# Optimization experiments

Measured on AMD Instinct MI355X. Metric: run time of the kernel, lower is better.

The kernel has to match this reference:

```python
import jax, jax.numpy as jnp
import numpy as np

BS = 15
NA = BS * BS
NOISE_SCALE = 2.0
TEMP = 0.03
VALUE_NOISE = 200.0

def _build_windows():
    # all length-5 windows in the 4 directions of a 15x15 board (572 total)
    wins = []
    for dr, dc in ((0, 1), (1, 0), (1, 1), (1, -1)):
        for r in range(BS):
            for c in range(BS):
                er, ec = r + 4 * dr, c + 4 * dc
                if 0 <= er < BS and 0 <= ec < BS:
                    wins.append([(r + k * dr) * BS + (c + k * dc) for k in range(5)])
    return np.asarray(wins, dtype=np.int32)

_WIN = _build_windows()                      # [572, 5] flat cell indices
_NW = _WIN.shape[0]
_Mnp = np.zeros((NA, _NW), dtype=np.float32)  # membership: cell i in window w
for w in range(_NW):
    _Mnp[_WIN[w], w] = 1.0
WIN_CELLS = jnp.asarray(_WIN)
MEMBER = jnp.asarray(_Mnp)                   # [225, 572]
WEIGHTS = jnp.asarray([0.0, 5.0, 50.0, 500.0, 5000.0, 100000.0], dtype=jnp.float32)

def _window_score(pc, oc):
    # matches _eval_board's per-window scoring table
    sp = jnp.where((oc == 0) & (pc > 0), WEIGHTS[jnp.minimum(pc, 5)], 0.0)
    so = jnp.where((pc == 0) & (oc > 0), WEIGHTS[jnp.minimum(oc, 5)], 0.0)
    return sp - so

def setup_inputs() -> dict:
    key = jax.random.key(0)
    k1, k2, k3, k4 = jax.random.split(key, 4)
    B = 8192
    boards = jax.random.randint(k1, (B, NA), 0, 3, dtype=jnp.int32)
    current_player = jax.random.randint(k2, (B,), 1, 3, dtype=jnp.int32)
    policy_noise = jax.random.normal(k3, (B, NA), dtype=jnp.float32)
    value_noise = jax.random.normal(k4, (B,), dtype=jnp.float32)
    return {"boards": boards, "current_player": current_player,
            "policy_noise": policy_noise, "value_noise": value_noise}

def reference(boards, current_player, policy_noise, value_noise):
    player = current_player[:, None, None]           # [B,1,1]
    opp = 3 - player
    cells = boards[:, WIN_CELLS]                      # [B, 572, 5]
    pc0 = jnp.sum(cells == player, axis=-1)           # [B, 572] player stones per window
    oc0 = jnp.sum(cells == opp, axis=-1)              # [B, 572] opponent stones per window
    s0 = _window_score(pc0, oc0)                      # base per-window score
    base = jnp.sum(s0, axis=-1)                       # [B] = _eval_board(board, player)
    # placing a player stone in an empty cell adds +1 to pc of every window containing it
    d = _window_score(pc0 + 1, oc0) - s0              # [B, 572]
    delta = jnp.einsum('bw,aw->ba', d, MEMBER)        # [B, 225]
    win_w = ((pc0 == 4) & (oc0 == 0)).astype(jnp.float32)
    win = jnp.einsum('bw,aw->ba', win_w, MEMBER) > 0  # [B, 225]
    empty = boards == 0
    logits = jnp.where(empty, jnp.where(win, 1e5, base[:, None] + delta), -1e6)
    valid = logits > -1e5                             # matches `logits > -100000.0`
    n = jnp.sum(valid, axis=-1).astype(jnp.float32)
    nsafe = jnp.maximum(n, 1.0)
    mean = jnp.sum(jnp.where(valid, logits, 0.0), axis=-1) / nsafe
    var = jnp.sum(jnp.where(valid, (logits - mean[:, None]) ** 2, 0.0), axis=-1) / nsafe
    std = jnp.maximum(1.0, jnp.sqrt(var))             # population std, floored at 1
    logits = logits + jnp.where(valid & (n[:, None] > 0),
                                policy_noise * NOISE_SCALE * std[:, None], 0.0)
    policy = jax.nn.softmax(logits * TEMP, axis=-1)   # [B, 225]
    value = jnp.clip(jnp.tanh((base + value_noise * VALUE_NOISE) / 3000.0), -0.95, 0.95)[:, None]
    return policy, value
```

## Files before the change

kernel.cpp:

```cpp
#include <hip/hip_runtime.h>
#include <math.h>

#define BSZ 15
#define NA  225
typedef unsigned long long u64;

__device__ __forceinline__ float wtab(int n) {
    return n == 1 ? 5.f : n == 2 ? 50.f : n == 3 ? 500.f : n == 4 ? 5000.f : 100000.f;
}
__device__ __forceinline__ float wredSum(float v) {
    #pragma unroll
    for (int off = 32; off; off >>= 1) v += __shfl_xor(v, off, 64);
    return v;
}
__device__ __forceinline__ float wredMax(float v) {
    #pragma unroll
    for (int off = 32; off; off >>= 1) v = fmaxf(v, __shfl_xor(v, off, 64));
    return v;
}

struct Masks { u64 P0, P1, P2, P3, O0, O1, O2, O3; };

template<int DIV, int CEXTRA, bool HAS64>
__device__ __forceinline__ void extractWin(int u, const Masks& M, u64 wmask,
                                           int& pc, int& oc)
{
    const int r = u / DIV;
    const int c = u % DIV + CEXTRA;
    const int idx = r * BSZ + c;
    const int q = idx >> 6, sh = idx & 63;
    const u64 Plo = (q & 2) ? ((q & 1) ? M.P3 : M.P2) : ((q & 1) ? M.P1 : M.P0);
    const u64 Phi = (q & 2) ? ((q & 1) ? 0ULL : M.P3) : ((q & 1) ? M.P2 : M.P1);
    const u64 Olo = (q & 2) ? ((q & 1) ? M.O3 : M.O2) : ((q & 1) ? M.O1 : M.O0);
    const u64 Ohi = (q & 2) ? ((q & 1) ? 0ULL : M.O3) : ((q & 1) ? M.O2 : M.O1);
    const u64 xP = (Plo >> sh) | ((Phi << (63 - sh)) << 1);
    const u64 xO = (Olo >> sh) | ((Ohi << (63 - sh)) << 1);
    pc = __popcll(xP & wmask);
    oc = __popcll(xO & wmask);
    if (HAS64) {
        pc += (int)((Phi >> sh) & 1ULL);
        oc += (int)((Ohi >> sh) & 1ULL);
    }
}

__device__ __forceinline__ void scoreD(int pc, int oc, float& s0, float& d) {
    const bool z_oc = (oc == 0), z_pc = (pc == 0);
    s0 = z_oc ? (z_pc ? 0.f : wtab(pc)) : (z_pc ? -wtab(oc) : 0.f);
    d  = (z_oc ? wtab(pc + 1) : 0.f) - s0;
}

__global__ __launch_bounds__(256, 4) void heur_kernel(
    const int* __restrict__ boards, const int* __restrict__ cur,
    const float* __restrict__ pnoise, const float* __restrict__ vnoise,
    float* __restrict__ out, int B)
{
    const int wid  = threadIdx.x >> 6;
    const int lane = threadIdx.x & 63;
    const int b    = blockIdx.x * 4 + wid;

    __shared__ float sDW[4][572];

    if (b >= B) return;

    float* __restrict__ dw = sDW[wid];

    const int player = cur[b];
    const int opp    = 3 - player;
    const int* __restrict__ gb = boards + (size_t)b * NA;

    const int v0 = gb[lane];
    const int v1 = gb[lane + 64];
    const int v2 = gb[lane + 128];
    const int v3 = (lane + 192 < NA) ? gb[lane + 192] : -1;

    const float* __restrict__ pn = pnoise + (size_t)b * NA;
    float pnv[4];
    pnv[0] = pn[lane];
    pnv[1] = pn[lane + 64];
    pnv[2] = pn[lane + 128];
    pnv[3] = (lane + 192 < NA) ? pn[lane + 192] : 0.f;
    const float vnb = vnoise[b];

    Masks M;
    M.P0 = __ballot(v0 == player); M.O0 = __ballot(v0 == opp);
    M.P1 = __ballot(v1 == player); M.O1 = __ballot(v1 == opp);
    M.P2 = __ballot(v2 == player); M.O2 = __ballot(v2 == opp);
    M.P3 = __ballot(v3 == player); M.O3 = __ballot(v3 == opp);

    const u64 MH = 0x1FULL;
    const u64 MV = 0x1000200040008001ULL;
    const u64 MD = 0x0001000100010001ULL;
    const u64 MA = 0x0100040010004001ULL;

    int pcS[10], ocS[10];
    const bool a2 = lane < 37, a7 = lane < 57;
    extractWin<11, 0, false>(lane,                 M, MH, pcS[0], ocS[0]);
    extractWin<11, 0, false>(lane + 64,            M, MH, pcS[1], ocS[1]);
    extractWin<11, 0, false>(min(lane + 128, 164), M, MH, pcS[2], ocS[2]);
    extractWin<15, 0, false>(lane,                 M, MV, pcS[3], ocS[3]);
    extractWin<15, 0, false>(lane + 64,            M, MV, pcS[4], ocS[4]);
    extractWin<15, 0, false>(min(lane + 128, 164), M, MV, pcS[5], ocS[5]);
    extractWin<11, 0, true >(lane,                 M, MD, pcS[6], ocS[6]);
    extractWin<11, 0, true >(min(lane + 64, 120),  M, MD, pcS[7], ocS[7]);
    extractWin<11, 4, false>(lane,                 M, MA, pcS[8], ocS[8]);
    extractWin<11, 4, false>(min(lane + 64, 120),  M, MA, pcS[9], ocS[9]);

    float baseLocal = 0.f;
    float s0v[10], dv[10];
    #pragma unroll
    for (int t = 0; t < 10; ++t) scoreD(pcS[t], ocS[t], s0v[t], dv[t]);
    const bool act[10] = {true, true, a2, true, true, a2, true, a7, true, a7};
    #pragma unroll
    for (int t = 0; t < 10; ++t) if (act[t]) baseLocal += s0v[t];

    dw[lane]             = dv[0];
    dw[lane + 64]        = dv[1];
    if (a2) dw[lane + 128] = dv[2];
    dw[165 + lane]       = dv[3];
    dw[165 + lane + 64]  = dv[4];
    if (a2) dw[165 + lane + 128] = dv[5];
    dw[330 + lane]       = dv[6];
    if (a7) dw[330 + lane + 64]  = dv[7];
    dw[451 + lane]       = dv[8];
    if (a7) dw[451 + lane + 64]  = dv[9];

    __threadfence_block();

    const float base = wredSum(baseLocal);

    const u64 C0 = M.P0 | M.O0, C1 = M.P1 | M.O1, C2 = M.P2 | M.O2, C3 = M.P3 | M.O3;

    float logitv[4];
    float nLoc = 0.f, sLoc = 0.f;
    #pragma unroll
    for (int j = 0; j < 4; ++j) {
        const int cl = lane + 64 * j;
        float lg = -1000000.f;
        if (cl < NA) {
            const int r = cl / BSZ, c = cl % BSZ;
            float acc = 0.f;
            bool  wf  = false;
            #pragma unroll
            for (int k = 0; k < 5; ++k) {
                const int wr = r - k;
                const int wcH = c - k;
                const int wcA = c + k - 4;
                const bool vR = (unsigned)wr  < 11u;
                const bool vH = (unsigned)wcH < 11u;
                const bool vA = (unsigned)wcA < 11u;
                if (vH)        { const float v = dw[r * 11 + wcH];          acc += v; wf |= (v == 95000.f); }
                if (vR)        { const float v = dw[165 + wr * 15 + c];     acc += v; wf |= (v == 95000.f); }
                if (vR && vH)  { const float v = dw[330 + wr * 11 + wcH];   acc += v; wf |= (v == 95000.f); }
                if (vR && vA)  { const float v = dw[451 + wr * 11 + wcA];   acc += v; wf |= (v == 95000.f); }
            }
            const u64 Cj = j == 0 ? C0 : j == 1 ? C1 : j == 2 ? C2 : C3;
            const bool isEmpty = ((Cj >> lane) & 1ULL) == 0ULL;
            if (isEmpty) lg = wf ? 100000.f : base + acc;
        }
        logitv[j] = lg;
        if (cl < NA && lg > -100000.f) { nLoc += 1.f; sLoc += lg; }
    }

    #pragma unroll
    for (int off = 32; off; off >>= 1) {
        nLoc += __shfl_xor(nLoc, off, 64);
        sLoc += __shfl_xor(sLoc, off, 64);
    }
    const float nsafe = fmaxf(nLoc, 1.f);
    const float mean  = sLoc / nsafe;

    float vLoc = 0.f;
    #pragma unroll
    for (int j = 0; j < 4; ++j) {
        const int cl = lane + 64 * j;
        if (cl < NA && logitv[j] > -100000.f) {
            const float dvv = logitv[j] - mean;
            vLoc += dvv * dvv;
        }
    }
    const float var  = wredSum(vLoc) / nsafe;
    const float std_ = fmaxf(1.f, sqrtf(var));
    const float nsc  = 2.0f * std_;
    const bool  anyValid = nLoc > 0.f;

    #pragma unroll
    for (int j = 0; j < 4; ++j) {
        const int cl = lane + 64 * j;
        if (cl < NA && logitv[j] > -100000.f && anyValid)
            logitv[j] += pnv[j] * nsc;
    }

    float xs[4];
    float mLoc = -INFINITY;
    #pragma unroll
    for (int j = 0; j < 4; ++j) {
        const int cl = lane + 64 * j;
        xs[j] = logitv[j] * 0.03f;
        if (cl < NA) mLoc = fmaxf(mLoc, xs[j]);
    }
    const float m = wredMax(mLoc);

    float ev[4];
    float eLoc = 0.f;
    #pragma unroll
    for (int j = 0; j < 4; ++j) {
        const int cl = lane + 64 * j;
        ev[j] = (cl < NA) ? __expf(xs[j] - m) : 0.f;
        eLoc += ev[j];
    }
    const float inv = 1.f / wredSum(eLoc);

    float* __restrict__ po = out + (size_t)b * NA;
    #pragma unroll
    for (int j = 0; j < 4; ++j) {
        const int cl = lane + 64 * j;
        if (cl < NA) po[cl] = ev[j] * inv;
    }

    if (lane == 0) {
        float v = tanhf((base + vnb * 200.0f) / 3000.0f);
        v = fminf(0.95f, fmaxf(-0.95f, v));
        out[(size_t)B * NA + b] = v;
    }
}

extern "C" void kernel_launch(void* const* d_in, const int* in_sizes, int n_in,
                              void* d_out, int out_size, void* d_ws, size_t ws_size,
                              hipStream_t stream) {
    const int*   boards = (const int*)d_in[0];
    const int*   cur    = (const int*)d_in[1];
    const float* pn     = (const float*)d_in[2];
    const float* vn     = (const float*)d_in[3];
    float*       outp   = (float*)d_out;
    const int B = in_sizes[1];

    const int grid = (B + 3) / 4;
    heur_kernel<<<grid, 256, 0, stream>>>(boards, cur, pn, vn, outp, B);
}
```

Before: 95.57 us.

## Process two boards per wavefront with interleaved independent work

Each wavefront now handles two boards instead of one. Window extraction, scoring, shared-memory gathers and all reductions are interleaved for the pair, and the grid is halved. This raises instruction-level parallelism, amortises index arithmetic and shuffle latency across two independent chains, and halves the number of waves launched. In exchange it raises register pressure and doubles shared memory per block, which can lower occupancy.

Result: slower. 102.7 us (+7.5%).

```diff
diff --git a/kernel.cpp b/kernel.cpp
--- a/kernel.cpp
+++ b/kernel.cpp
@@ -8,31 +8,17 @@
 __device__ __forceinline__ float wtab(int n) {
     return n == 1 ? 5.f : n == 2 ? 50.f : n == 3 ? 500.f : n == 4 ? 5000.f : 100000.f;
 }
-__device__ __forceinline__ float wredSum(float v) {
-    #pragma unroll
-    for (int off = 32; off; off >>= 1) v += __shfl_xor(v, off, 64);
-    return v;
-}
-__device__ __forceinline__ float wredMax(float v) {
-    #pragma unroll
-    for (int off = 32; off; off >>= 1) v = fmaxf(v, __shfl_xor(v, off, 64));
-    return v;
-}
-
-struct Masks { u64 P0, P1, P2, P3, O0, O1, O2, O3; };
-
-template<int DIV, int CEXTRA, bool HAS64>
-__device__ __forceinline__ void extractWin(int u, const Masks& M, u64 wmask,
-                                           int& pc, int& oc)
+
+struct Masks { u64 P[4], O[4]; };
+
+template<bool HAS64>
+__device__ __forceinline__ void extract2(int q, int sh, const Masks& M, u64 wmask,
+                                         int& pc, int& oc)
 {
-    const int r = u / DIV;
-    const int c = u % DIV + CEXTRA;
-    const int idx = r * BSZ + c;
-    const int q = idx >> 6, sh = idx & 63;
-    const u64 Plo = (q & 2) ? ((q & 1) ? M.P3 : M.P2) : ((q & 1) ? M.P1 : M.P0);
-    const u64 Phi = (q & 2) ? ((q & 1) ? 0ULL : M.P3) : ((q & 1) ? M.P2 : M.P1);
-    const u64 Olo = (q & 2) ? ((q & 1) ? M.O3 : M.O2) : ((q & 1) ? M.O1 : M.O0);
-    const u64 Ohi = (q & 2) ? ((q & 1) ? 0ULL : M.O3) : ((q & 1) ? M.O2 : M.O1);
+    const u64 Plo = (q & 2) ? ((q & 1) ? M.P[3] : M.P[2]) : ((q & 1) ? M.P[1] : M.P[0]);
+    const u64 Phi = (q & 2) ? ((q & 1) ? 0ULL   : M.P[3]) : ((q & 1) ? M.P[2] : M.P[1]);
+    const u64 Olo = (q & 2) ? ((q & 1) ? M.O[3] : M.O[2]) : ((q & 1) ? M.O[1] : M.O[0]);
+    const u64 Ohi = (q & 2) ? ((q & 1) ? 0ULL   : M.O[3]) : ((q & 1) ? M.O[2] : M.O[1]);
     const u64 xP = (Plo >> sh) | ((Phi << (63 - sh)) << 1);
     const u64 xO = (Olo >> sh) | ((Ohi << (63 - sh)) << 1);
     pc = __popcll(xP & wmask);
@@ -49,6 +35,29 @@
     d  = (z_oc ? wtab(pc + 1) : 0.f) - s0;
 }
 
+template<int DIV, int CEXTRA, bool HAS64>
+__device__ __forceinline__ void doSlot2(int u, bool act, u64 wmask, int toff,
+                                        const Masks& M0, const Masks& M1,
+                                        float* __restrict__ dw0, float* __restrict__ dw1,
+                                        float& base0, float& base1)
+{
+    const int r = u / DIV;
+    const int c = u % DIV + CEXTRA;
+    const int idx = r * BSZ + c;
+    const int q = idx >> 6, sh = idx & 63;
+    int pc0, oc0, pc1, oc1;
+    extract2<HAS64>(q, sh, M0, wmask, pc0, oc0);
+    extract2<HAS64>(q, sh, M1, wmask, pc1, oc1);
+    float s00, d0, s01, d1;
+    scoreD(pc0, oc0, s00, d0);
+    scoreD(pc1, oc1, s01, d1);
+    if (act) {
+        base0 += s00; base1 += s01;
+        dw0[toff + u] = d0;
+        dw1[toff + u] = d1;
+    }
+}
+
 __global__ __launch_bounds__(256, 4) void heur_kernel(
     const int* __restrict__ boards, const int* __restrict__ cur,
     const float* __restrict__ pnoise, const float* __restrict__ vnoise,
@@ -56,171 +65,201 @@
 {
     const int wid  = threadIdx.x >> 6;
     const int lane = threadIdx.x & 63;
-    const int b    = blockIdx.x * 4 + wid;
-
-    __shared__ float sDW[4][572];
-
-    if (b >= B) return;
-
-    float* __restrict__ dw = sDW[wid];
-
-    const int player = cur[b];
-    const int opp    = 3 - player;
-    const int* __restrict__ gb = boards + (size_t)b * NA;
-
-    const int v0 = gb[lane];
-    const int v1 = gb[lane + 64];
-    const int v2 = gb[lane + 128];
-    const int v3 = (lane + 192 < NA) ? gb[lane + 192] : -1;
-
-    const float* __restrict__ pn = pnoise + (size_t)b * NA;
-    float pnv[4];
-    pnv[0] = pn[lane];
-    pnv[1] = pn[lane + 64];
-    pnv[2] = pn[lane + 128];
-    pnv[3] = (lane + 192 < NA) ? pn[lane + 192] : 0.f;
-    const float vnb = vnoise[b];
-
-    Masks M;
-    M.P0 = __ballot(v0 == player); M.O0 = __ballot(v0 == opp);
-    M.P1 = __ballot(v1 == player); M.O1 = __ballot(v1 == opp);
-    M.P2 = __ballot(v2 == player); M.O2 = __ballot(v2 == opp);
-    M.P3 = __ballot(v3 == player); M.O3 = __ballot(v3 == opp);
+    const int bb   = blockIdx.x * 8 + wid * 2;
+
+    __shared__ float sDW[8][572];
+
+    if (bb >= B) return;
+    const bool b1ok = (bb + 1 < B);
+    const int  b0 = bb, b1 = b1ok ? bb + 1 : bb;
+
+    float* __restrict__ dw0 = sDW[wid * 2];
+    float* __restrict__ dw1 = sDW[wid * 2 + 1];
+
+    const int pl0 = cur[b0], op0 = 3 - pl0;
+    const int pl1 = cur[b1], op1 = 3 - pl1;
+    const int* __restrict__ gb0 = boards + (size_t)b0 * NA;
+    const int* __restrict__ gb1 = boards + (size_t)b1 * NA;
+
+    int v0[4], v1[4];
+    v0[0] = gb0[lane]; v0[1] = gb0[lane + 64]; v0[2] = gb0[lane + 128];
+    v0[3] = (lane + 192 < NA) ? gb0[lane + 192] : -1;
+    v1[0] = gb1[lane]; v1[1] = gb1[lane + 64]; v1[2] = gb1[lane + 128];
+    v1[3] = (lane + 192 < NA) ? gb1[lane + 192] : -1;
+
+    const float* __restrict__ pn0 = pnoise + (size_t)b0 * NA;
+    const float* __restrict__ pn1 = pnoise + (size_t)b1 * NA;
+    float pnv0[4], pnv1[4];
+    pnv0[0] = pn0[lane]; pnv0[1] = pn0[lane + 64]; pnv0[2] = pn0[lane + 128];
+    pnv0[3] = (lane + 192 < NA) ? pn0[lane + 192] : 0.f;
+    pnv1[0] = pn1[lane]; pnv1[1] = pn1[lane + 64]; pnv1[2] = pn1[lane + 128];
+    pnv1[3] = (lane + 192 < NA) ? pn1[lane + 192] : 0.f;
+    const float vnb0 = vnoise[b0], vnb1 = vnoise[b1];
+
+    Masks M0, M1;
+    #pragma unroll
+    for (int k = 0; k < 4; ++k) {
+        M0.P[k] = __ballot(v0[k] == pl0); M0.O[k] = __ballot(v0[k] == op0);
+        M1.P[k] = __ballot(v1[k] == pl1); M1.O[k] = __ballot(v1[k] == op1);
+    }
+    u64 C0[4], C1[4];
+    #pragma unroll
+    for (int k = 0; k < 4; ++k) { C0[k] = M0.P[k] | M0.O[k]; C1[k] = M1.P[k] | M1.O[k]; }
 
     const u64 MH = 0x1FULL;
     const u64 MV = 0x1000200040008001ULL;
     const u64 MD = 0x0001000100010001ULL;
     const u64 MA = 0x0100040010004001ULL;
-
-    int pcS[10], ocS[10];
     const bool a2 = lane < 37, a7 = lane < 57;
-    extractWin<11, 0, false>(lane,                 M, MH, pcS[0], ocS[0]);
-    extractWin<11, 0, false>(lane + 64,            M, MH, pcS[1], ocS[1]);
-    extractWin<11, 0, false>(min(lane + 128, 164), M, MH, pcS[2], ocS[2]);
-    extractWin<15, 0, false>(lane,                 M, MV, pcS[3], ocS[3]);
-    extractWin<15, 0, false>(lane + 64,            M, MV, pcS[4], ocS[4]);
-    extractWin<15, 0, false>(min(lane + 128, 164), M, MV, pcS[5], ocS[5]);
-    extractWin<11, 0, true >(lane,                 M, MD, pcS[6], ocS[6]);
-    extractWin<11, 0, true >(min(lane + 64, 120),  M, MD, pcS[7], ocS[7]);
-    extractWin<11, 4, false>(lane,                 M, MA, pcS[8], ocS[8]);
-    extractWin<11, 4, false>(min(lane + 64, 120),  M, MA, pcS[9], ocS[9]);
-
-    float baseLocal = 0.f;
-    float s0v[10], dv[10];
-    #pragma unroll
-    for (int t = 0; t < 10; ++t) scoreD(pcS[t], ocS[t], s0v[t], dv[t]);
-    const bool act[10] = {true, true, a2, true, true, a2, true, a7, true, a7};
-    #pragma unroll
-    for (int t = 0; t < 10; ++t) if (act[t]) baseLocal += s0v[t];
-
-    dw[lane]             = dv[0];
-    dw[lane + 64]        = dv[1];
-    if (a2) dw[lane + 128] = dv[2];
-    dw[165 + lane]       = dv[3];
-    dw[165 + lane + 64]  = dv[4];
-    if (a2) dw[165 + lane + 128] = dv[5];
-    dw[330 + lane]       = dv[6];
-    if (a7) dw[330 + lane + 64]  = dv[7];
-    dw[451 + lane]       = dv[8];
-    if (a7) dw[451 + lane + 64]  = dv[9];
+
+    float base0 = 0.f, base1 = 0.f;
+    doSlot2<11, 0, false>(lane,                 true, MH, 0,   M0, M1, dw0, dw1, base0, base1);
+    doSlot2<11, 0, false>(lane + 64,            true, MH, 0,   M0, M1, dw0, dw1, base0, base1);
+    doSlot2<11, 0, false>(min(lane + 128, 164), a2,   MH, 0,   M0, M1, dw0, dw1, base0, base1);
+    doSlot2<15, 0, false>(lane,                 true, MV, 165, M0, M1, dw0, dw1, base0, base1);
+    doSlot2<15, 0, false>(lane + 64,            true, MV, 165, M0, M1, dw0, dw1, base0, base1);
+    doSlot2<15, 0, false>(min(lane + 128, 164), a2,   MV, 165, M0, M1, dw0, dw1, base0, base1);
+    doSlot2<11, 0, true >(lane,                 true, MD, 330, M0, M1, dw0, dw1, base0, base1);
+    doSlot2<11, 0, true >(min(lane + 64, 120),  a7,   MD, 330, M0, M1, dw0, dw1, base0, base1);
+    doSlot2<11, 4, false>(lane,                 true, MA, 451, M0, M1, dw0, dw1, base0, base1);
+    doSlot2<11, 4, false>(min(lane + 64, 120),  a7,   MA, 451, M0, M1, dw0, dw1, base0, base1);
 
     __threadfence_block();
 
-    const float base = wredSum(baseLocal);
-
-    const u64 C0 = M.P0 | M.O0, C1 = M.P1 | M.O1, C2 = M.P2 | M.O2, C3 = M.P3 | M.O3;
-
-    float logitv[4];
-    float nLoc = 0.f, sLoc = 0.f;
-    #pragma unroll
-    for (int j = 0; j < 4; ++j) {
-        const int cl = lane + 64 * j;
-        float lg = -1000000.f;
+    #pragma unroll
+    for (int off = 32; off; off >>= 1) {
+        base0 += __shfl_xor(base0, off, 64);
+        base1 += __shfl_xor(base1, off, 64);
+    }
+
+    float lg0[4], lg1[4];
+    float n0 = 0.f, s0 = 0.f, n1 = 0.f, s1 = 0.f;
+    #pragma unroll
+    for (int j = 0; j < 4; ++j) {
+        const int cl = lane + 64 * j;
+        float a0 = 0.f, a1 = 0.f;
+        bool  w0 = false, w1 = false;
+        float l0 = -1000000.f, l1 = -1000000.f;
         if (cl < NA) {
             const int r = cl / BSZ, c = cl % BSZ;
-            float acc = 0.f;
-            bool  wf  = false;
             #pragma unroll
             for (int k = 0; k < 5; ++k) {
-                const int wr = r - k;
+                const int wr  = r - k;
                 const int wcH = c - k;
                 const int wcA = c + k - 4;
                 const bool vR = (unsigned)wr  < 11u;
                 const bool vH = (unsigned)wcH < 11u;
                 const bool vA = (unsigned)wcA < 11u;
-                if (vH)        { const float v = dw[r * 11 + wcH];          acc += v; wf |= (v == 95000.f); }
-                if (vR)        { const float v = dw[165 + wr * 15 + c];     acc += v; wf |= (v == 95000.f); }
-                if (vR && vH)  { const float v = dw[330 + wr * 11 + wcH];   acc += v; wf |= (v == 95000.f); }
-                if (vR && vA)  { const float v = dw[451 + wr * 11 + wcA];   acc += v; wf |= (v == 95000.f); }
+                if (vH) {
+                    const int i = r * 11 + wcH;
+                    const float x0 = dw0[i], x1 = dw1[i];
+                    a0 += x0; w0 |= (x0 == 95000.f);
+                    a1 += x1; w1 |= (x1 == 95000.f);
+                }
+                if (vR) {
+                    const int i = 165 + wr * 15 + c;
+                    const float x0 = dw0[i], x1 = dw1[i];
+                    a0 += x0; w0 |= (x0 == 95000.f);
+                    a1 += x1; w1 |= (x1 == 95000.f);
+                }
+                if (vR && vH) {
+                    const int i = 330 + wr * 11 + wcH;
+                    const float x0 = dw0[i], x1 = dw1[i];
+                    a0 += x0; w0 |= (x0 == 95000.f);
+                    a1 += x1; w1 |= (x1 == 95000.f);
+                }
+                if (vR && vA) {
+                    const int i = 451 + wr * 11 + wcA;
+                    const float x0 = dw0[i], x1 = dw1[i];
+                    a0 += x0; w0 |= (x0 == 95000.f);
+                    a1 += x1; w1 |= (x1 == 95000.f);
+                }
             }
-            const u64 Cj = j == 0 ? C0 : j == 1 ? C1 : j == 2 ? C2 : C3;
-            const bool isEmpty = ((Cj >> lane) & 1ULL) == 0ULL;
-            if (isEmpty) lg = wf ? 100000.f : base + acc;
+            const u64 c0 = j == 0 ? C0[0] : j == 1 ? C0[1] : j == 2 ? C0[2] : C0[3];
+            const u64 c1 = j == 0 ? C1[0] : j == 1 ? C1[1] : j == 2 ? C1[2] : C1[3];
+            if (((c0 >> lane) & 1ULL) == 0ULL) l0 = w0 ? 100000.f : base0 + a0;
+            if (((c1 >> lane) & 1ULL) == 0ULL) l1 = w1 ? 100000.f : base1 + a1;
         }
-        logitv[j] = lg;
-        if (cl < NA && lg > -100000.f) { nLoc += 1.f; sLoc += lg; }
-    }
-
-    #pragma unroll
-    for (int off = 32; off; off >>= 1) {
-        nLoc += __shfl_xor(nLoc, off, 64);
-        sLoc += __shfl_xor(sLoc, off, 64);
-    }
-    const float nsafe = fmaxf(nLoc, 1.f);
-    const float mean  = sLoc / nsafe;
-
-    float vLoc = 0.f;
-    #pragma unroll
-    for (int j = 0; j < 4; ++j) {
-        const int cl = lane + 64 * j;
-        if (cl < NA && logitv[j] > -100000.f) {
-            const float dvv = logitv[j] - mean;
-            vLoc += dvv * dvv;
+        lg0[j] = l0; lg1[j] = l1;
+        if (cl < NA && l0 > -100000.f) { n0 += 1.f; s0 += l0; }
+        if (cl < NA && l1 > -100000.f) { n1 += 1.f; s1 += l1; }
+    }
+
+    #pragma unroll
+    for (int off = 32; off; off >>= 1) {
+        n0 += __shfl_xor(n0, off, 64); s0 += __shfl_xor(s0, off, 64);
+        n1 += __shfl_xor(n1, off, 64); s1 += __shfl_xor(s1, off, 64);
+    }
+    const float mean0 = s0 / fmaxf(n0, 1.f);
+    const float mean1 = s1 / fmaxf(n1, 1.f);
+
+    float q0 = 0.f, q1 = 0.f;
+    #pragma unroll
+    for (int j = 0; j < 4; ++j) {
+        const int cl = lane + 64 * j;
+        if (cl < NA && lg0[j] > -100000.f) { const float d = lg0[j] - mean0; q0 += d * d; }
+        if (cl < NA && lg1[j] > -100000.f) { const float d = lg1[j] - mean1; q1 += d * d; }
+    }
+    #pragma unroll
+    for (int off = 32; off; off >>= 1) {
+        q0 += __shfl_xor(q0, off, 64);
+        q1 += __shfl_xor(q1, off, 64);
+    }
+    const float nsc0 = 2.0f * fmaxf(1.f, sqrtf(q0 / fmaxf(n0, 1.f)));
+    const float nsc1 = 2.0f * fmaxf(1.f, sqrtf(q1 / fmaxf(n1, 1.f)));
+    const bool av0 = n0 > 0.f, av1 = n1 > 0.f;
+
+    float xs0[4], xs1[4];
+    float m0 = -INFINITY, m1 = -INFINITY;
+    #pragma unroll
+    for (int j = 0; j < 4; ++j) {
+        const int cl = lane + 64 * j;
+        float l0 = lg0[j], l1 = lg1[j];
+        if (cl < NA && l0 > -100000.f && av0) l0 += pnv0[j] * nsc0;
+        if (cl < NA && l1 > -100000.f && av1) l1 += pnv1[j] * nsc1;
+        xs0[j] = l0 * 0.03f; xs1[j] = l1 * 0.03f;
+        if (cl < NA) { m0 = fmaxf(m0, xs0[j]); m1 = fmaxf(m1, xs1[j]); }
+    }
+    #pragma unroll
+    for (int off = 32; off; off >>= 1) {
+        m0 = fmaxf(m0, __shfl_xor(m0, off, 64));
+        m1 = fmaxf(m1, __shfl_xor(m1, off, 64));
+    }
+
+    float ev0[4], ev1[4];
+    float e0 = 0.f, e1 = 0.f;
+    #pragma unroll
+    for (int j = 0; j < 4; ++j) {
+        const int cl = lane + 64 * j;
+        ev0[j] = (cl < NA) ? __expf(xs0[j] - m0) : 0.f;
+        ev1[j] = (cl < NA) ? __expf(xs1[j] - m1) : 0.f;
+        e0 += ev0[j]; e1 += ev1[j];
+    }
+    #pragma unroll
+    for (int off = 32; off; off >>= 1) {
+        e0 += __shfl_xor(e0, off, 64);
+        e1 += __shfl_xor(e1, off, 64);
+    }
+    const float inv0 = 1.f / e0, inv1 = 1.f / e1;
+
+    float* __restrict__ po0 = out + (size_t)b0 * NA;
+    float* __restrict__ po1 = out + (size_t)b1 * NA;
+    #pragma unroll
+    for (int j = 0; j < 4; ++j) {
+        const int cl = lane + 64 * j;
+        if (cl < NA) {
+            po0[cl] = ev0[j] * inv0;
+            if (b1ok) po1[cl] = ev1[j] * inv1;
         }
     }
-    const float var  = wredSum(vLoc) / nsafe;
-    const float std_ = fmaxf(1.f, sqrtf(var));
-    const float nsc  = 2.0f * std_;
-    const bool  anyValid = nLoc > 0.f;
-
-    #pragma unroll
-    for (int j = 0; j < 4; ++j) {
-        const int cl = lane + 64 * j;
-        if (cl < NA && logitv[j] > -100000.f && anyValid)
-            logitv[j] += pnv[j] * nsc;
-    }
-
-    float xs[4];
-    float mLoc = -INFINITY;
-    #pragma unroll
-    for (int j = 0; j < 4; ++j) {
-        const int cl = lane + 64 * j;
-        xs[j] = logitv[j] * 0.03f;
-        if (cl < NA) mLoc = fmaxf(mLoc, xs[j]);
-    }
-    const float m = wredMax(mLoc);
-
-    float ev[4];
-    float eLoc = 0.f;
-    #pragma unroll
-    for (int j = 0; j < 4; ++j) {
-        const int cl = lane + 64 * j;
-        ev[j] = (cl < NA) ? __expf(xs[j] - m) : 0.f;
-        eLoc += ev[j];
-    }
-    const float inv = 1.f / wredSum(eLoc);
-
-    float* __restrict__ po = out + (size_t)b * NA;
-    #pragma unroll
-    for (int j = 0; j < 4; ++j) {
-        const int cl = lane + 64 * j;
-        if (cl < NA) po[cl] = ev[j] * inv;
-    }
 
     if (lane == 0) {
-        float v = tanhf((base + vnb * 200.0f) / 3000.0f);
-        v = fminf(0.95f, fmaxf(-0.95f, v));
-        out[(size_t)B * NA + b] = v;
+        float w = tanhf((base0 + vnb0 * 200.0f) / 3000.0f);
+        out[(size_t)B * NA + b0] = fminf(0.95f, fmaxf(-0.95f, w));
+        if (b1ok) {
+            float y = tanhf((base1 + vnb1 * 200.0f) / 3000.0f);
+            out[(size_t)B * NA + b1] = fminf(0.95f, fmaxf(-0.95f, y));
+        }
     }
 }
 
@@ -234,6 +273,6 @@
     float*       outp   = (float*)d_out;
     const int B = in_sizes[1];
 
-    const int grid = (B + 3) / 4;
+    const int grid = (B + 7) / 8;
     heur_kernel<<<grid, 256, 0, stream>>>(boards, cur, pn, vn, outp, B);
 }
```
